# Kernel optimization log

Measured on AMD Instinct MI355X. Metric: run time of the kernel, lower is better.

## Reference

```python
import jax, jax.numpy as jnp
import numpy as np

S, B, D, H, FF = 1024, 8, 512, 8, 2048
HD = D // H
ALPHA, BETA = 0.5, 0.5
EPS = 1e-5


def setup_inputs() -> dict:
    key = jax.random.key(0)
    ks = jax.random.split(key, 12)
    rn = lambda k, sh, sc=0.02: jax.random.normal(k, sh, dtype=jnp.float32) * sc
    ln = jnp.stack([jnp.ones(D), jnp.zeros(D), jnp.ones(D), jnp.zeros(D)]).astype(jnp.float32)
    return {
        "src": rn(ks[0], (S, B, D), 1.0),
        "src_depth": rn(ks[1], (S, B, D), 1.0),
        "pos": rn(ks[2], (S, B, D), 1.0),
        "attn_w_img": rn(ks[3], (4, D, D)),
        "attn_b_img": jnp.zeros((4, D), jnp.float32),
        "attn_w_dpt": rn(ks[4], (4, D, D)),
        "attn_b_dpt": jnp.zeros((4, D), jnp.float32),
        "ffn_w1_img": rn(ks[5], (FF, D)),
        "ffn_b1_img": jnp.zeros((FF,), jnp.float32),
        "ffn_w2_img": rn(ks[6], (D, FF)),
        "ffn_b2_img": jnp.zeros((D,), jnp.float32),
        "ffn_w1_dpt": rn(ks[7], (FF, D)),
        "ffn_b1_dpt": jnp.zeros((FF,), jnp.float32),
        "ffn_w2_dpt": rn(ks[8], (D, FF)),
        "ffn_b2_dpt": jnp.zeros((D,), jnp.float32),
        "ln_img": ln,
        "ln_dpt": ln,
    }


def _layer_norm(x, g, b):
    m = jnp.mean(x, axis=-1, keepdims=True)
    v = jnp.var(x, axis=-1, keepdims=True)  # biased, matches torch LayerNorm
    return (x - m) * jax.lax.rsqrt(v + EPS) * g + b


def _heads(t, W, b):  # [B,S,D] x [D,D] -> [B,H,S,hd]  (torch Linear: y = x W^T + b)
    y = jnp.einsum('bsd,ed->bse', t, W) + b
    return y.reshape(B, S, H, HD).transpose(0, 2, 1, 3)


def _forward(src, src_depth, pos, attn_w_img, attn_b_img, attn_w_dpt, attn_b_dpt,
             ffn_w1_img, ffn_b1_img, ffn_w2_img, ffn_b2_img,
             ffn_w1_dpt, ffn_b1_dpt, ffn_w2_dpt, ffn_b2_dpt, ln_img, ln_dpt):
    # seq-first -> batch-first
    x = src.transpose(1, 0, 2)        # [B,S,D]
    xd = src_depth.transpose(1, 0, 2)
    p = pos.transpose(1, 0, 2)
    qk_in = x + p                     # img stream: q = k = src + pos
    # depth stream: pos_depth is None in layer.forward -> no pos embed
    q = _heads(qk_in, attn_w_img[0], attn_b_img[0])
    k = _heads(qk_in, attn_w_img[1], attn_b_img[1])
    v = _heads(x, attn_w_img[2], attn_b_img[2])
    qd = _heads(xd, attn_w_dpt[0], attn_b_dpt[0])
    kd = _heads(xd, attn_w_dpt[1], attn_b_dpt[1])
    vd = _heads(xd, attn_w_dpt[2], attn_b_dpt[2])
    scale = 1.0 / np.sqrt(HD).astype(np.float32)
    a_img = jax.nn.softmax(jnp.einsum('bhld,bhsd->bhls', q, k) * scale, axis=-1)
    a_dpt = jax.nn.softmax(jnp.einsum('bhld,bhsd->bhls', qd, kd) * scale, axis=-1)
    sh_img = (1.0 - ALPHA) * a_img + ALPHA * a_dpt
    sh_dpt = (1.0 - BETA) * a_dpt + BETA * a_img
    o_img = jnp.einsum('bhls,bhsd->bhld', sh_img, v).transpose(0, 2, 1, 3).reshape(B, S, D)
    o_dpt = jnp.einsum('bhls,bhsd->bhld', sh_dpt, vd).transpose(0, 2, 1, 3).reshape(B, S, D)
    o_img = jnp.einsum('bsd,ed->bse', o_img, attn_w_img[3]) + attn_b_img[3]
    o_dpt = jnp.einsum('bsd,ed->bse', o_dpt, attn_w_dpt[3]) + attn_b_dpt[3]
    # img residual + LN + FFN + LN
    x = _layer_norm(x + o_img, ln_img[0], ln_img[1])
    ff = jnp.einsum('bsf,df->bsd',
                    jax.nn.relu(jnp.einsum('bsd,fd->bsf', x, ffn_w1_img) + ffn_b1_img),
                    ffn_w2_img) + ffn_b2_img
    x = _layer_norm(x + ff, ln_img[2], ln_img[3])
    # depth residual + LN + FFN + LN
    xd = _layer_norm(xd + o_dpt, ln_dpt[0], ln_dpt[1])
    ffd = jnp.einsum('bsf,df->bsd',
                     jax.nn.relu(jnp.einsum('bsd,fd->bsf', xd, ffn_w1_dpt) + ffn_b1_dpt),
                     ffn_w2_dpt) + ffn_b2_dpt
    xd = _layer_norm(xd + ffd, ln_dpt[2], ln_dpt[3])
    return x.transpose(1, 0, 2), xd.transpose(1, 0, 2)  # back to [S,B,D]


def reference(src, src_depth, pos, attn_w_img, attn_b_img, attn_w_dpt, attn_b_dpt,
              ffn_w1_img, ffn_b1_img, ffn_w2_img, ffn_b2_img,
              ffn_w1_dpt, ffn_b1_dpt, ffn_w2_dpt, ffn_b2_dpt, ln_img, ln_dpt):
    return _forward(src, src_depth, pos, attn_w_img, attn_b_img, attn_w_dpt, attn_b_dpt,
                    ffn_w1_img, ffn_b1_img, ffn_w2_img, ffn_b2_img,
                    ffn_w1_dpt, ffn_b1_dpt, ffn_w2_dpt, ffn_b2_dpt, ln_img, ln_dpt)
```

## Files before the change

### kernel.cpp

```cpp
#include <hip/hip_runtime.h>
#include <math.h>

#define S_  1024
#define B_  8
#define D_  512
#define H_  8
#define HD_ 64
#define FF_ 2048
#define M_  8192
#define DD_ (D_ * D_)

typedef __attribute__((ext_vector_type(8))) short short8;
typedef __attribute__((ext_vector_type(4))) float f32x4;

static __device__ __forceinline__ unsigned short f2bf(float x) {
  union { float f; unsigned int u; } v; v.f = x;
  unsigned int r = v.u + 0x7fff + ((v.u >> 16) & 1);
  return (unsigned short)(r >> 16);
}
static __device__ __forceinline__ float bf2f(unsigned short x) {
  union { unsigned int u; float f; } v; v.u = ((unsigned int)x) << 16;
  return v.f;
}
static __device__ __forceinline__ unsigned int pack_bf2(float a, float b) {
  union { float f; unsigned int u; } x, y; x.f = a; y.f = b;
  return ((x.u + 0x8000u) >> 16) | ((y.u + 0x8000u) & 0xffff0000u);
}
static __device__ __forceinline__ void gl_lds16(const unsigned short* g, unsigned short* l) {
  __builtin_amdgcn_global_load_lds((__attribute__((address_space(1))) void*)(g),
                                   (__attribute__((address_space(3))) void*)(l), 16, 0, 0);
}
static __device__ __forceinline__ int xcd_swz(int phys, int nwg) {
  int cpx = nwg >> 3;
  return (phys & 7) * cpx + (phys >> 3);
}

struct CvtJobs { const float* in[6]; unsigned short* out[6]; };
__global__ __launch_bounds__(256) void wcvt_kernel(CvtJobs j) {
  int job = blockIdx.y;
  int i = (blockIdx.x * 256 + threadIdx.x) * 4;
  float4 v = *(const float4*)(j.in[job] + i);
  unsigned short u[4] = {f2bf(v.x), f2bf(v.y), f2bf(v.z), f2bf(v.w)};
  *(uint2*)(j.out[job] + i) = *(const uint2*)u;
}

__global__ __launch_bounds__(256) void acvt_kernel(const float* __restrict__ src,
    const float* __restrict__ srcd, const float* __restrict__ pos,
    unsigned short* __restrict__ src16, unsigned short* __restrict__ srcd16,
    unsigned short* __restrict__ qkin16) {
  int job = blockIdx.y;
  int i = (blockIdx.x * 256 + threadIdx.x) * 4;
  const float* a = (job == 0) ? src : (job == 1) ? srcd : src;
  float4 v = *(const float4*)(a + i);
  if (job == 2) {
    float4 p = *(const float4*)(pos + i);
    v.x += p.x; v.y += p.y; v.z += p.z; v.w += p.w;
  }
  unsigned short* o = (job == 0) ? src16 : (job == 1) ? srcd16 : qkin16;
  unsigned short u[4] = {f2bf(v.x), f2bf(v.y), f2bf(v.z), f2bf(v.w)};
  *(uint2*)(o + i) = *(const uint2*)u;
}

static __device__ __forceinline__ void mgemm_body(
    const unsigned short* __restrict__ X, const unsigned short* __restrict__ W,
    const float* __restrict__ bias, const float* __restrict__ resf,
    const unsigned short* __restrict__ resb, unsigned short* __restrict__ Yb,
    float* __restrict__ Yf, int N, int K, int relu, int bx, int by,
    unsigned short* As, unsigned short* Bs)
{
  int tid = threadIdx.x;
  int lane = tid & 63, w = tid >> 6;
  int ml = lane & 15, g = lane >> 4;
  int wm = w >> 1, wn = w & 1;
  int m0 = by * 128, n0 = bx * 128;
  int mxs = (ml >> 1) & 3;

  int lrow = tid >> 2;
  int sg = (tid & 3) ^ ((lrow >> 1) & 3);
  const unsigned short* gA = X + (size_t)(m0 + lrow) * K + sg * 8;
  const unsigned short* gB = W + (size_t)(n0 + lrow) * K + sg * 8;
  unsigned short* lA = As + w * 512;
  unsigned short* lB = Bs + w * 512;

  f32x4 acc[4][4];
  #pragma unroll
  for (int i = 0; i < 4; i++)
    #pragma unroll
    for (int j = 0; j < 4; j++) acc[i][j] = (f32x4){0.f, 0.f, 0.f, 0.f};

  int NT = K >> 5;

  auto STAGE = [&](int buf, int kt) {
    const unsigned short* ga = gA + kt * 32;
    const unsigned short* gb = gB + kt * 32;
    unsigned short* la = lA + buf * 4096;
    unsigned short* lb = lB + buf * 4096;
    gl_lds16(ga, la);
    gl_lds16(ga + (size_t)64 * K, la + 2048);
    gl_lds16(gb, lb);
    gl_lds16(gb + (size_t)64 * K, lb + 2048);
  };

  STAGE(0, 0);
  __syncthreads();

  for (int kt = 0; kt < NT; kt++) {
    int cur = kt & 1;
    if (kt + 1 < NT) STAGE(cur ^ 1, kt + 1);

    const unsigned short* lAc = As + cur * 4096;
    const unsigned short* lBc = Bs + cur * 4096;
    short8 af[4], bfr[4];
    #pragma unroll
    for (int i = 0; i < 4; i++) {
      int r = wm * 64 + i * 16 + ml;
      af[i] = *(const short8*)&lAc[r * 32 + ((g ^ mxs) * 8)];
    }
    #pragma unroll
    for (int j = 0; j < 4; j++) {
      int r = wn * 64 + j * 16 + ml;
      bfr[j] = *(const short8*)&lBc[r * 32 + ((g ^ mxs) * 8)];
    }
    #pragma unroll
    for (int i = 0; i < 4; i++)
      #pragma unroll
      for (int j = 0; j < 4; j++)
        acc[i][j] = __builtin_amdgcn_mfma_f32_16x16x32_bf16(af[i], bfr[j], acc[i][j], 0, 0, 0);

    __syncthreads();
  }

  #pragma unroll
  for (int i = 0; i < 4; i++) {
    int grow = m0 + wm * 64 + i * 16 + g * 4;
    #pragma unroll
    for (int j = 0; j < 4; j++) {
      int gcol = n0 + wn * 64 + j * 16 + ml;
      float bv = bias[gcol];
      #pragma unroll
      for (int r = 0; r < 4; r++) {
        size_t idx = (size_t)(grow + r) * N + gcol;
        float v = acc[i][j][r] + bv;
        if (resf) v += resf[idx];
        if (resb) v += bf2f(resb[idx]);
        if (relu) v = fmaxf(v, 0.0f);
        if (Yb) Yb[idx] = f2bf(v);
        if (Yf) Yf[idx] = v;
      }
    }
  }
}

__global__ __launch_bounds__(256, 4) void qkv_kernel(
    const unsigned short* __restrict__ qkin, const unsigned short* __restrict__ src16,
    const unsigned short* __restrict__ srcd16,
    const unsigned short* __restrict__ w_i, const unsigned short* __restrict__ w_d,
    const float* __restrict__ bA_i, const float* __restrict__ bA_d,
    unsigned short* __restrict__ qkimg, unsigned short* __restrict__ vimg,
    unsigned short* __restrict__ dptqkv)
{
  __shared__ unsigned short As[2 * 128 * 32];
  __shared__ unsigned short Bs[2 * 128 * 32];
  int phys = blockIdx.x + 24 * blockIdx.y;
  int L = xcd_swz(phys, 24 * 64);
  int bx = L % 24, by = L / 24;
  if (bx < 8)
    mgemm_body(qkin, w_i, bA_i, nullptr, nullptr, qkimg, nullptr, 1024, 512, 0, bx, by, As, Bs);
  else if (bx < 12)
    mgemm_body(src16, w_i + 2 * DD_, bA_i + 1024, nullptr, nullptr, vimg, nullptr, 512, 512, 0, bx - 8, by, As, Bs);
  else
    mgemm_body(srcd16, w_d, bA_d, nullptr, nullptr, dptqkv, nullptr, 1536, 512, 0, bx - 12, by, As, Bs);
}

__global__ __launch_bounds__(256, 4) void pgemm_kernel(
    const unsigned short* __restrict__ X0, const unsigned short* __restrict__ X1,
    const unsigned short* __restrict__ W0, const unsigned short* __restrict__ W1,
    const float* __restrict__ b0, const float* __restrict__ b1,
    const float* __restrict__ rf0, const float* __restrict__ rf1,
    const unsigned short* __restrict__ rb0, const unsigned short* __restrict__ rb1,
    unsigned short* __restrict__ Y0, unsigned short* __restrict__ Y1,
    int N, int K, int relu)
{
  __shared__ unsigned short As[2 * 128 * 32];
  __shared__ unsigned short Bs[2 * 128 * 32];
  int nbx = gridDim.x;
  int nwg = nbx * 64 * 2;
  int phys = blockIdx.x + nbx * (blockIdx.y + 64 * blockIdx.z);
  int L = xcd_swz(phys, nwg);
  int bx = L % nbx; int rem = L / nbx;
  int by = rem % 64; int z = rem / 64;
  mgemm_body(z ? X1 : X0, z ? W1 : W0, z ? b1 : b0, z ? rf1 : rf0,
             z ? rb1 : rb0, z ? Y1 : Y0, nullptr, N, K, relu,
             bx, by, As, Bs);
}

__global__ __launch_bounds__(256) void vtrans_kernel(
    const unsigned short* __restrict__ v0, int ld0, unsigned short* __restrict__ vt0,
    const unsigned short* __restrict__ v1, int ld1, unsigned short* __restrict__ vt1)
{
  __shared__ unsigned short tile[64][72];
  const unsigned short* v = blockIdx.z ? v1 : v0;
  unsigned short* vt = blockIdx.z ? vt1 : vt0;
  int ld = blockIdx.z ? ld1 : ld0;
  int bh = blockIdx.y, b = bh >> 3, h = bh & 7;
  int s0 = blockIdx.x * 64;
  int tid = threadIdx.x;
  #pragma unroll
  for (int t = 0; t < 2; t++) {
    int idx = t * 256 + tid;
    int i = idx >> 3, c8 = (idx & 7) * 8;
    *(uint4*)&tile[i][c8] =
        *(const uint4*)(v + ((size_t)(s0 + i) * B_ + b) * ld + h * HD_ + c8);
  }
  __syncthreads();
  int hd = tid >> 2, j0 = (tid & 3) * 16;
  unsigned short tmp[16];
  #pragma unroll
  for (int j = 0; j < 16; j++) tmp[j] = tile[j0 + j][hd];
  unsigned short* dst = vt + ((size_t)bh * HD_ + hd) * S_ + s0 + j0;
  *(uint4*)(dst) = *(const uint4*)&tmp[0];
  *(uint4*)(dst + 8) = *(const uint4*)&tmp[8];
}

__global__ __launch_bounds__(256) void ln16_kernel(
    const unsigned short* __restrict__ X0, const unsigned short* __restrict__ X1,
    unsigned short* __restrict__ Yb0, unsigned short* __restrict__ Yb1,
    float* __restrict__ Yf0, float* __restrict__ Yf1,
    const float* __restrict__ gb0, const float* __restrict__ gb1)
{
  int row = blockIdx.x, tid = threadIdx.x;
  int strm = row >> 13, r = row & 8191;
  const unsigned short* X = strm ? X1 : X0;
  unsigned short* Yb = strm ? Yb1 : Yb0;
  float* Yf = strm ? Yf1 : Yf0;
  const float* gb = strm ? gb1 : gb0;

  ushort2 xv = *(const ushort2*)(X + (size_t)r * D_ + 2 * tid);
  float v0 = bf2f(xv.x), v1 = bf2f(xv.y);
  float s = v0 + v1, q = v0 * v0 + v1 * v1;
  #pragma unroll
  for (int msk = 1; msk < 64; msk <<= 1) {
    s += __shfl_xor(s, msk);
    q += __shfl_xor(q, msk);
  }
  __shared__ float ss[4], qs[4];
  int wid = tid >> 6;
  if ((tid & 63) == 0) { ss[wid] = s; qs[wid] = q; }
  __syncthreads();
  s = ss[0] + ss[1] + ss[2] + ss[3];
  q = qs[0] + qs[1] + qs[2] + qs[3];
  float mean = s * (1.0f / D_);
  float var  = q * (1.0f / D_) - mean * mean;
  float inv  = rsqrtf(var + 1e-5f);
  float2 gg = *(const float2*)(gb + 2 * tid);
  float2 bb = *(const float2*)(gb + 512 + 2 * tid);
  float o0 = (v0 - mean) * inv * gg.x + bb.x;
  float o1 = (v1 - mean) * inv * gg.y + bb.y;
  if (Yb) {
    unsigned short u[2] = {f2bf(o0), f2bf(o1)};
    *(unsigned int*)(Yb + (size_t)r * D_ + 2 * tid) = *(const unsigned int*)u;
  }
  if (Yf) {
    float2 o; o.x = o0; o.y = o1;
    *(float2*)(Yf + (size_t)r * D_ + 2 * tid) = o;
  }
}

__global__ __launch_bounds__(256, 2) void attn_kernel(
    const unsigned short* __restrict__ Qi, const unsigned short* __restrict__ Ki, int ldi,
    const unsigned short* __restrict__ Vti,
    const unsigned short* __restrict__ Qd, const unsigned short* __restrict__ Kd, int ldd,
    const unsigned short* __restrict__ Vtd,
    unsigned short* __restrict__ oi, unsigned short* __restrict__ od)
{
  __shared__ __align__(16) unsigned short Kls[2][64 * 64];
  __shared__ __align__(16) unsigned short Vls[2][64 * 64];
  __shared__ __align__(16) unsigned short Pl[4][2][16 * 72];

  int tid = threadIdx.x;
  int phys = blockIdx.x + 8 * blockIdx.y;
  int L = xcd_swz(phys, 8 * 64);
  int bh = L >> 3, b = bh >> 3, h = bh & 7;
  int q0 = (L & 7) * 128;
  int lane = tid & 63, w = tid >> 6;
  int ml = lane & 15, g = lane >> 4;
  int mx = ml & 7;

  short8 qf[2][2][2];
  #pragma unroll
  for (int t = 0; t < 2; t++) {
    size_t tok = (size_t)(q0 + w * 32 + t * 16 + ml) * B_ + b;
    const unsigned short* qa_i = Qi + tok * ldi + h * HD_ + g * 8;
    const unsigned short* qa_d = Qd + tok * ldd + h * HD_ + g * 8;
    qf[t][0][0] = *(const short8*)(qa_i);  qf[t][0][1] = *(const short8*)(qa_i + 32);
    qf[t][1][0] = *(const short8*)(qa_d);  qf[t][1][1] = *(const short8*)(qa_d + 32);
  }

  int srow = lane >> 3;
  int chg = (lane & 7) ^ srow;
  const unsigned short* gbase; size_t s1, s2; unsigned short* lbase;
  if (w == 0)      { gbase = Ki  + ((size_t)srow * B_ + b) * ldi + h * HD_ + chg * 8; s1 = (size_t)B_ * ldi; s2 = s1; lbase = &Kls[0][0]; }
  else if (w == 1) { gbase = Kd  + ((size_t)srow * B_ + b) * ldd + h * HD_ + chg * 8; s1 = (size_t)B_ * ldd; s2 = s1; lbase = &Kls[1][0]; }
  else if (w == 2) { gbase = Vti + (size_t)bh * HD_ * S_ + (size_t)srow * S_ + chg * 8; s1 = S_; s2 = 1; lbase = &Vls[0][0]; }
  else             { gbase = Vtd + (size_t)bh * HD_ * S_ + (size_t)srow * S_ + chg * 8; s1 = S_; s2 = 1; lbase = &Vls[1][0]; }

  f32x4 acc4[2][4][4];
  #pragma unroll
  for (int t = 0; t < 2; t++)
    #pragma unroll
    for (int cb = 0; cb < 4; cb++)
      #pragma unroll
      for (int n = 0; n < 4; n++) acc4[t][cb][n] = (f32x4){0.f, 0.f, 0.f, 0.f};
  float lI[2] = {0.f, 0.f}, lD[2] = {0.f, 0.f};
  const float scale = 0.125f;

  for (int kt = 0; kt < S_ / 64; kt++) {
    int k0 = kt * 64;
    __syncthreads();
    {
      const unsigned short* gp = gbase + (size_t)k0 * s2;
      #pragma unroll
      for (int rr = 0; rr < 8; rr++)
        gl_lds16(gp + (size_t)rr * 8 * s1, lbase + rr * 512);
    }
    __syncthreads();

    #pragma unroll
    for (int t = 0; t < 2; t++) {
      #pragma unroll
      for (int st = 0; st < 2; st++) {
        float* ls = st ? &lD[t] : &lI[t];
        const unsigned short* Kt = &Kls[st][0];
        #pragma unroll
        for (int n = 0; n < 4; n++) {
          int rbase = (n * 16 + ml) * 64;
          short8 kf0 = *(const short8*)&Kt[rbase + ((g ^ mx) * 8)];
          short8 kf1 = *(const short8*)&Kt[rbase + (((g + 4) ^ mx) * 8)];
          f32x4 a = (f32x4){0.f, 0.f, 0.f, 0.f};
          a = __builtin_amdgcn_mfma_f32_16x16x32_bf16(kf0, qf[t][st][0], a, 0, 0, 0);
          a = __builtin_amdgcn_mfma_f32_16x16x32_bf16(kf1, qf[t][st][1], a, 0, 0, 0);
          float p0 = __expf(a[0] * scale), p1 = __expf(a[1] * scale);
          float p2 = __expf(a[2] * scale), p3 = __expf(a[3] * scale);
          *ls += (p0 + p1) + (p2 + p3);
          uint2 pk; pk.x = pack_bf2(p0, p1); pk.y = pack_bf2(p2, p3);
          *(uint2*)&Pl[w][st][ml * 72 + n * 16 + g * 4] = pk;
        }
      }
      #pragma unroll
      for (int c = 0; c < 2; c++) {
        short8 pI = *(const short8*)&Pl[w][0][ml * 72 + g * 8 + c * 32];
        short8 pD = *(const short8*)&Pl[w][1][ml * 72 + g * 8 + c * 32];
        #pragma unroll
        for (int n = 0; n < 4; n++) {
          int rbase = (n * 16 + ml) * 64;
          int sc = (((g + 4 * c) ^ mx)) * 8;
          short8 vI = *(const short8*)&Vls[0][rbase + sc];
          short8 vD = *(const short8*)&Vls[1][rbase + sc];
          acc4[t][0][n] = __builtin_amdgcn_mfma_f32_16x16x32_bf16(pI, vI, acc4[t][0][n], 0, 0, 0);
          acc4[t][1][n] = __builtin_amdgcn_mfma_f32_16x16x32_bf16(pD, vI, acc4[t][1][n], 0, 0, 0);
          acc4[t][2][n] = __builtin_amdgcn_mfma_f32_16x16x32_bf16(pI, vD, acc4[t][2][n], 0, 0, 0);
          acc4[t][3][n] = __builtin_amdgcn_mfma_f32_16x16x32_bf16(pD, vD, acc4[t][3][n], 0, 0, 0);
        }
      }
    }
  }

  #pragma unroll
  for (int t = 0; t < 2; t++) {
    lI[t] += __shfl_xor(lI[t], 16);  lI[t] += __shfl_xor(lI[t], 32);
    lD[t] += __shfl_xor(lD[t], 16);  lD[t] += __shfl_xor(lD[t], 32);
  }
  #pragma unroll
  for (int t = 0; t < 2; t++) {
    float invI = 1.0f / lI[t], invD = 1.0f / lD[t];
    #pragma unroll
    for (int r = 0; r < 4; r++) {
      float iI = __shfl(invI, g * 4 + r, 16);
      float iD = __shfl(invD, g * 4 + r, 16);
      int qrow = q0 + w * 32 + t * 16 + g * 4 + r;
      size_t ob = ((size_t)qrow * B_ + b) * D_ + h * HD_;
      #pragma unroll
      for (int n = 0; n < 4; n++) {
        oi[ob + n * 16 + ml] = f2bf(0.5f * (acc4[t][0][n][r] * iI + acc4[t][1][n][r] * iD));
        od[ob + n * 16 + ml] = f2bf(0.5f * (acc4[t][3][n][r] * iD + acc4[t][2][n][r] * iI));
      }
    }
  }
}

extern "C" void kernel_launch(void* const* d_in, const int* in_sizes, int n_in,
                              void* d_out, int out_size, void* d_ws, size_t ws_size,
                              hipStream_t stream) {
  const float* src  = (const float*)d_in[0];
  const float* srcd = (const float*)d_in[1];
  const float* pos  = (const float*)d_in[2];
  const float* wA_i = (const float*)d_in[3];
  const float* bA_i = (const float*)d_in[4];
  const float* wA_d = (const float*)d_in[5];
  const float* bA_d = (const float*)d_in[6];
  const float* w1_i = (const float*)d_in[7];
  const float* b1_i = (const float*)d_in[8];
  const float* w2_i = (const float*)d_in[9];
  const float* b2_i = (const float*)d_in[10];
  const float* w1_d = (const float*)d_in[11];
  const float* b1_d = (const float*)d_in[12];
  const float* w2_d = (const float*)d_in[13];
  const float* b2_d = (const float*)d_in[14];
  const float* ln_i = (const float*)d_in[15];
  const float* ln_d = (const float*)d_in[16];

  float* out = (float*)d_out;
  unsigned short* u = (unsigned short*)d_ws;
  const size_t T4 = (size_t)M_ * D_;
  const size_t WSZ = (size_t)FF_ * D_;

  unsigned short* src16  = u;
  unsigned short* srcd16 = u + T4;
  unsigned short* qkimg  = u + 2 * T4;
  unsigned short* vimg   = u + 4 * T4;
  unsigned short* dptqkv = u + 5 * T4;
  unsigned short* w_i16  = u + 8 * T4;
  unsigned short* w_d16  = w_i16 + WSZ;
  unsigned short* w1i16  = w_d16 + WSZ;
  unsigned short* w2i16  = w1i16 + WSZ;
  unsigned short* w1d16  = w2i16 + WSZ;
  unsigned short* w2d16  = w1d16 + WSZ;
  unsigned short* t16_i  = w2d16 + WSZ;
  unsigned short* t16_d  = t16_i + T4;
  unsigned short* x16_i  = t16_d + T4;
  unsigned short* x16_d  = x16_i + T4;
  unsigned short* vt_i   = src16;
  unsigned short* vt_d   = srcd16;
  unsigned short* h16_i  = u;
  unsigned short* h16_d  = u + 4 * T4;
  unsigned short* qkin16 = (unsigned short*)out;
  unsigned short* oi16   = (unsigned short*)out;
  unsigned short* od16   = (unsigned short*)out + T4;

  dim3 blk(256);

  CvtJobs cj;
  cj.in[0] = wA_i; cj.out[0] = w_i16;
  cj.in[1] = wA_d; cj.out[1] = w_d16;
  cj.in[2] = w1_i; cj.out[2] = w1i16;
  cj.in[3] = w2_i; cj.out[3] = w2i16;
  cj.in[4] = w1_d; cj.out[4] = w1d16;
  cj.in[5] = w2_d; cj.out[5] = w2d16;
  wcvt_kernel<<<dim3(1024, 6), blk, 0, stream>>>(cj);
  acvt_kernel<<<dim3(4096, 3), blk, 0, stream>>>(src, srcd, pos, src16, srcd16, qkin16);

  qkv_kernel<<<dim3(24, 64), blk, 0, stream>>>(qkin16, src16, srcd16, w_i16, w_d16,
                                               bA_i, bA_d, qkimg, vimg, dptqkv);
  vtrans_kernel<<<dim3(16, 64, 2), blk, 0, stream>>>(vimg, 512, vt_i, dptqkv + 1024, 1536, vt_d);

  attn_kernel<<<dim3(S_ / 128, B_ * H_), blk, 0, stream>>>(
      qkimg, qkimg + 512, 1024, vt_i, dptqkv, dptqkv + 512, 1536, vt_d, oi16, od16);

  pgemm_kernel<<<dim3(4, 64, 2), blk, 0, stream>>>(
      oi16, od16, w_i16 + 3 * DD_, w_d16 + 3 * DD_, bA_i + 1536, bA_d + 1536,
      src, srcd, nullptr, nullptr, t16_i, t16_d, 512, 512, 0);
  ln16_kernel<<<2 * M_, blk, 0, stream>>>(t16_i, t16_d, x16_i, x16_d,
                                          nullptr, nullptr, ln_i, ln_d);
  pgemm_kernel<<<dim3(16, 64, 2), blk, 0, stream>>>(
      x16_i, x16_d, w1i16, w1d16, b1_i, b1_d,
      nullptr, nullptr, nullptr, nullptr, h16_i, h16_d, 2048, 512, 1);
  pgemm_kernel<<<dim3(4, 64, 2), blk, 0, stream>>>(
      h16_i, h16_d, w2i16, w2d16, b2_i, b2_d,
      nullptr, nullptr, x16_i, x16_d, t16_i, t16_d, 512, 2048, 0);
  ln16_kernel<<<2 * M_, blk, 0, stream>>>(t16_i, t16_d, nullptr, nullptr,
                                          out, out + T4, ln_i + 2 * D_, ln_d + 2 * D_);
}
```

Measured before the change: 434.2 us.

## Merge conversion kernels, use one wave per LayerNorm row, prioritize MFMA in attention

Merges the weight and activation bf16 conversion kernels into a single launch that selects its job from a flat block index. Rewrites the LayerNorm kernel so one wavefront handles a whole row with 16-byte vector loads, which removes the shared-memory reduction and the block barrier and cuts the block count by four. Wraps the attention MFMA groups in s_setprio calls to raise wave priority while issuing matrix ops. These are three separate tweaks aimed at launch overhead, memory access width and instruction scheduling.

```diff
diff --git a/kernel.cpp b/kernel.cpp
--- a/kernel.cpp
+++ b/kernel.cpp
@@ -35,30 +35,32 @@
   return (phys & 7) * cpx + (phys >> 3);
 }
 
-struct CvtJobs { const float* in[6]; unsigned short* out[6]; };
-__global__ __launch_bounds__(256) void wcvt_kernel(CvtJobs j) {
-  int job = blockIdx.y;
-  int i = (blockIdx.x * 256 + threadIdx.x) * 4;
-  float4 v = *(const float4*)(j.in[job] + i);
-  unsigned short u[4] = {f2bf(v.x), f2bf(v.y), f2bf(v.z), f2bf(v.w)};
-  *(uint2*)(j.out[job] + i) = *(const uint2*)u;
-}
-
-__global__ __launch_bounds__(256) void acvt_kernel(const float* __restrict__ src,
-    const float* __restrict__ srcd, const float* __restrict__ pos,
-    unsigned short* __restrict__ src16, unsigned short* __restrict__ srcd16,
-    unsigned short* __restrict__ qkin16) {
-  int job = blockIdx.y;
-  int i = (blockIdx.x * 256 + threadIdx.x) * 4;
-  const float* a = (job == 0) ? src : (job == 1) ? srcd : src;
-  float4 v = *(const float4*)(a + i);
-  if (job == 2) {
-    float4 p = *(const float4*)(pos + i);
-    v.x += p.x; v.y += p.y; v.z += p.z; v.w += p.w;
-  }
-  unsigned short* o = (job == 0) ? src16 : (job == 1) ? srcd16 : qkin16;
-  unsigned short u[4] = {f2bf(v.x), f2bf(v.y), f2bf(v.z), f2bf(v.w)};
-  *(uint2*)(o + i) = *(const uint2*)u;
+struct CvtArgs {
+  const float* win[6]; unsigned short* wout[6];
+  const float* src; const float* srcd; const float* pos;
+  unsigned short* src16; unsigned short* srcd16; unsigned short* qkin16;
+};
+__global__ __launch_bounds__(256) void cvt_kernel(CvtArgs a) {
+  int bid = blockIdx.x;
+  if (bid < 12288) {
+    int job = bid >> 12, bx = bid & 4095;
+    int i = (bx * 256 + threadIdx.x) * 4;
+    const float* in = (job == 0) ? a.src : (job == 1) ? a.srcd : a.src;
+    float4 v = *(const float4*)(in + i);
+    if (job == 2) {
+      float4 p = *(const float4*)(a.pos + i);
+      v.x += p.x; v.y += p.y; v.z += p.z; v.w += p.w;
+    }
+    unsigned short* o = (job == 0) ? a.src16 : (job == 1) ? a.srcd16 : a.qkin16;
+    unsigned short u[4] = {f2bf(v.x), f2bf(v.y), f2bf(v.z), f2bf(v.w)};
+    *(uint2*)(o + i) = *(const uint2*)u;
+  } else {
+    int wjob = (bid - 12288) >> 10, bx = (bid - 12288) & 1023;
+    int i = (bx * 256 + threadIdx.x) * 4;
+    float4 v = *(const float4*)(a.win[wjob] + i);
+    unsigned short u[4] = {f2bf(v.x), f2bf(v.y), f2bf(v.z), f2bf(v.w)};
+    *(uint2*)(a.wout[wjob] + i) = *(const uint2*)u;
+  }
 }
 
 static __device__ __forceinline__ void mgemm_body(
@@ -228,41 +230,49 @@
     float* __restrict__ Yf0, float* __restrict__ Yf1,
     const float* __restrict__ gb0, const float* __restrict__ gb1)
 {
-  int row = blockIdx.x, tid = threadIdx.x;
-  int strm = row >> 13, r = row & 8191;
+  int tid = threadIdx.x;
+  int w = tid >> 6, lane = tid & 63;
+  int R = blockIdx.x * 4 + w;
+  int strm = R >> 13, r = R & 8191;
   const unsigned short* X = strm ? X1 : X0;
   unsigned short* Yb = strm ? Yb1 : Yb0;
   float* Yf = strm ? Yf1 : Yf0;
   const float* gb = strm ? gb1 : gb0;
 
-  ushort2 xv = *(const ushort2*)(X + (size_t)r * D_ + 2 * tid);
-  float v0 = bf2f(xv.x), v1 = bf2f(xv.y);
-  float s = v0 + v1, q = v0 * v0 + v1 * v1;
+  short8 xv = *(const short8*)(X + (size_t)r * D_ + lane * 8);
+  float v[8];
+  #pragma unroll
+  for (int j = 0; j < 8; j++) v[j] = bf2f((unsigned short)xv[j]);
+  float s = 0.f, q = 0.f;
+  #pragma unroll
+  for (int j = 0; j < 8; j++) { s += v[j]; q += v[j] * v[j]; }
   #pragma unroll
   for (int msk = 1; msk < 64; msk <<= 1) {
     s += __shfl_xor(s, msk);
     q += __shfl_xor(q, msk);
   }
-  __shared__ float ss[4], qs[4];
-  int wid = tid >> 6;
-  if ((tid & 63) == 0) { ss[wid] = s; qs[wid] = q; }
-  __syncthreads();
-  s = ss[0] + ss[1] + ss[2] + ss[3];
-  q = qs[0] + qs[1] + qs[2] + qs[3];
   float mean = s * (1.0f / D_);
   float var  = q * (1.0f / D_) - mean * mean;
   float inv  = rsqrtf(var + 1e-5f);
-  float2 gg = *(const float2*)(gb + 2 * tid);
-  float2 bb = *(const float2*)(gb + 512 + 2 * tid);
-  float o0 = (v0 - mean) * inv * gg.x + bb.x;
-  float o1 = (v1 - mean) * inv * gg.y + bb.y;
+  float4 g0 = *(const float4*)(gb + lane * 8);
+  float4 g1 = *(const float4*)(gb + lane * 8 + 4);
+  float4 b0 = *(const float4*)(gb + 512 + lane * 8);
+  float4 b1 = *(const float4*)(gb + 512 + lane * 8 + 4);
+  float gg[8] = {g0.x, g0.y, g0.z, g0.w, g1.x, g1.y, g1.z, g1.w};
+  float bb[8] = {b0.x, b0.y, b0.z, b0.w, b1.x, b1.y, b1.z, b1.w};
+  float o[8];
+  #pragma unroll
+  for (int j = 0; j < 8; j++) o[j] = (v[j] - mean) * inv * gg[j] + bb[j];
   if (Yb) {
-    unsigned short u[2] = {f2bf(o0), f2bf(o1)};
-    *(unsigned int*)(Yb + (size_t)r * D_ + 2 * tid) = *(const unsigned int*)u;
+    unsigned short u[8];
+    #pragma unroll
+    for (int j = 0; j < 8; j++) u[j] = f2bf(o[j]);
+    *(uint4*)(Yb + (size_t)r * D_ + lane * 8) = *(const uint4*)u;
   }
   if (Yf) {
-    float2 o; o.x = o0; o.y = o1;
-    *(float2*)(Yf + (size_t)r * D_ + 2 * tid) = o;
+    float* dst = Yf + (size_t)r * D_ + lane * 8;
+    *(float4*)(dst)     = (float4){o[0], o[1], o[2], o[3]};
+    *(float4*)(dst + 4) = (float4){o[4], o[5], o[6], o[7]};
   }
 }
 
@@ -337,8 +347,10 @@
           short8 kf0 = *(const short8*)&Kt[rbase + ((g ^ mx) * 8)];
           short8 kf1 = *(const short8*)&Kt[rbase + (((g + 4) ^ mx) * 8)];
           f32x4 a = (f32x4){0.f, 0.f, 0.f, 0.f};
+          __builtin_amdgcn_s_setprio(1);
           a = __builtin_amdgcn_mfma_f32_16x16x32_bf16(kf0, qf[t][st][0], a, 0, 0, 0);
           a = __builtin_amdgcn_mfma_f32_16x16x32_bf16(kf1, qf[t][st][1], a, 0, 0, 0);
+          __builtin_amdgcn_s_setprio(0);
           float p0 = __expf(a[0] * scale), p1 = __expf(a[1] * scale);
           float p2 = __expf(a[2] * scale), p3 = __expf(a[3] * scale);
           *ls += (p0 + p1) + (p2 + p3);
@@ -356,10 +368,12 @@
           int sc = (((g + 4 * c) ^ mx)) * 8;
           short8 vI = *(const short8*)&Vls[0][rbase + sc];
           short8 vD = *(const short8*)&Vls[1][rbase + sc];
+          __builtin_amdgcn_s_setprio(1);
           acc4[t][0][n] = __builtin_amdgcn_mfma_f32_16x16x32_bf16(pI, vI, acc4[t][0][n], 0, 0, 0);
           acc4[t][1][n] = __builtin_amdgcn_mfma_f32_16x16x32_bf16(pD, vI, acc4[t][1][n], 0, 0, 0);
           acc4[t][2][n] = __builtin_amdgcn_mfma_f32_16x16x32_bf16(pI, vD, acc4[t][2][n], 0, 0, 0);
           acc4[t][3][n] = __builtin_amdgcn_mfma_f32_16x16x32_bf16(pD, vD, acc4[t][3][n], 0, 0, 0);
+          __builtin_amdgcn_s_setprio(0);
         }
       }
     }
@@ -439,15 +453,16 @@
 
   dim3 blk(256);
 
-  CvtJobs cj;
-  cj.in[0] = wA_i; cj.out[0] = w_i16;
-  cj.in[1] = wA_d; cj.out[1] = w_d16;
-  cj.in[2] = w1_i; cj.out[2] = w1i16;
-  cj.in[3] = w2_i; cj.out[3] = w2i16;
-  cj.in[4] = w1_d; cj.out[4] = w1d16;
-  cj.in[5] = w2_d; cj.out[5] = w2d16;
-  wcvt_kernel<<<dim3(1024, 6), blk, 0, stream>>>(cj);
-  acvt_kernel<<<dim3(4096, 3), blk, 0, stream>>>(src, srcd, pos, src16, srcd16, qkin16);
+  CvtArgs ca;
+  ca.win[0] = wA_i; ca.wout[0] = w_i16;
+  ca.win[1] = wA_d; ca.wout[1] = w_d16;
+  ca.win[2] = w1_i; ca.wout[2] = w1i16;
+  ca.win[3] = w2_i; ca.wout[3] = w2i16;
+  ca.win[4] = w1_d; ca.wout[4] = w1d16;
+  ca.win[5] = w2_d; ca.wout[5] = w2d16;
+  ca.src = src; ca.srcd = srcd; ca.pos = pos;
+  ca.src16 = src16; ca.srcd16 = srcd16; ca.qkin16 = qkin16;
+  cvt_kernel<<<dim3(18432), blk, 0, stream>>>(ca);
 
   qkv_kernel<<<dim3(24, 64), blk, 0, stream>>>(qkin16, src16, srcd16, w_i16, w_d16,
                                                bA_i, bA_d, qkimg, vimg, dptqkv);
@@ -459,14 +474,14 @@
   pgemm_kernel<<<dim3(4, 64, 2), blk, 0, stream>>>(
       oi16, od16, w_i16 + 3 * DD_, w_d16 + 3 * DD_, bA_i + 1536, bA_d + 1536,
       src, srcd, nullptr, nullptr, t16_i, t16_d, 512, 512, 0);
-  ln16_kernel<<<2 * M_, blk, 0, stream>>>(t16_i, t16_d, x16_i, x16_d,
-                                          nullptr, nullptr, ln_i, ln_d);
+  ln16_kernel<<<dim3(2 * M_ / 4), blk, 0, stream>>>(t16_i, t16_d, x16_i, x16_d,
+                                                    nullptr, nullptr, ln_i, ln_d);
   pgemm_kernel<<<dim3(16, 64, 2), blk, 0, stream>>>(
       x16_i, x16_d, w1i16, w1d16, b1_i, b1_d,
       nullptr, nullptr, nullptr, nullptr, h16_i, h16_d, 2048, 512, 1);
   pgemm_kernel<<<dim3(4, 64, 2), blk, 0, stream>>>(
       h16_i, h16_d, w2i16, w2d16, b2_i, b2_d,
       nullptr, nullptr, x16_i, x16_d, t16_i, t16_d, 512, 2048, 0);
-  ln16_kernel<<<2 * M_, blk, 0, stream>>>(t16_i, t16_d, nullptr, nullptr,
-                                          out, out + T4, ln_i + 2 * D_, ln_d + 2 * D_);
-}
+  ln16_kernel<<<dim3(2 * M_ / 4), blk, 0, stream>>>(t16_i, t16_d, nullptr, nullptr,
+                                                    out, out + T4, ln_i + 2 * D_, ln_d + 2 * D_);
+}
```

Result: faster. 416.1 us (median of 2 runs) (-4.2%).
